# Kernel optimization log

Hardware: AMD Instinct MI355X
Metric: run time of the kernel (lower is better)

Reference implementation:

```python
import jax, jax.numpy as jnp
import numpy as np
import math

N_RES, N_EDGE = 10000, 320000
C_S, C_Z, C_H, H, PQ, PV = 384, 128, 16, 12, 4, 8
INF, EPS = 1e5, 1e-8


def _lin(key, din, dout):
    k1, k2 = jax.random.split(key)
    w = jax.random.normal(k1, (din, dout), jnp.float32) * (1.0 / np.sqrt(din))
    b = jax.random.normal(k2, (dout,), jnp.float32) * 0.02
    return w, b


def setup_inputs() -> dict:
    key = jax.random.key(0)
    ks = jax.random.split(key, 16)
    s = jax.random.normal(ks[0], (N_RES, C_S), jnp.float32)
    z = jax.random.normal(ks[1], (N_EDGE, C_Z), jnp.float32)
    edge_index = jax.random.randint(ks[2], (2, N_EDGE), 0, N_RES, jnp.int32)
    rot = jnp.linalg.qr(jax.random.normal(ks[3], (N_RES, 3, 3), jnp.float32))[0]
    trans = jax.random.normal(ks[4], (N_RES, 3), jnp.float32)
    mask = jnp.ones((N_RES,), jnp.float32)
    wq, bq = _lin(ks[5], C_S, H * C_H)
    wkv, bkv = _lin(ks[6], C_S, 2 * H * C_H)
    wqp, bqp = _lin(ks[7], C_S, H * PQ * 3)
    wkvp, bkvp = _lin(ks[8], C_S, H * (PQ + PV) * 3)
    wb, bb = _lin(ks[9], C_Z, H)
    wdz, bdz = _lin(ks[10], C_Z, C_Z // 4)
    head_w = jax.random.normal(ks[11], (H,), jnp.float32) * 0.1
    wout, bout = _lin(ks[12], H * (C_Z // 4 + C_H + PV * 4), C_S)
    return dict(s=s, z=z, rot=rot, trans=trans, mask=mask, edge_index=edge_index,
                wq=wq, bq=bq, wkv=wkv, bkv=bkv, wqp=wqp, bqp=bqp, wkvp=wkvp, bkvp=bkvp,
                wb=wb, bb=bb, wdz=wdz, bdz=bdz, head_w=head_w, wout=wout, bout=bout)


def reference(s, z, rot, trans, mask, edge_index, wq, bq, wkv, bkv, wqp, bqp,
              wkvp, bkvp, wb, bb, wdz, bdz, head_w, wout, bout):
    n = s.shape[0]
    src, dst = edge_index[0], edge_index[1]  # key-side, query-side

    q = (s @ wq + bq).reshape(n, H, C_H)
    kv = (s @ wkv + bkv).reshape(n, H, 2 * C_H)
    k, v = kv[..., :C_H], kv[..., C_H:]

    def make_pts(x, p):
        # torch: split [n, H*p*3] into 3 chunks of H*p, stack on last dim -> [n, H*p, 3]
        x = jnp.stack(jnp.split(x, 3, axis=-1), axis=-1)
        x = jnp.einsum('nij,npj->npi', rot, x) + trans[:, None, :]  # global frame
        return x.reshape(n, H, p, 3)

    q_pts = make_pts(s @ wqp + bqp, PQ)                 # [n, H, PQ, 3]
    kv_pts = make_pts(s @ wkvp + bkvp, PQ + PV)
    k_pts, v_pts = kv_pts[..., :PQ, :], kv_pts[..., PQ:, :]

    b = z @ wb + bb                                      # [E, H]
    a = jnp.einsum('ehc,ehc->eh', q[dst], k[src]) * math.sqrt(1.0 / (3 * C_H))
    a = a + math.sqrt(1.0 / 3) * b

    disp = q_pts[dst] - k_pts[src]                       # [E, H, PQ, 3]
    hw = jax.nn.softplus(head_w) * math.sqrt(1.0 / (3 * (PQ * 9.0 / 2)))
    pt_att = -0.5 * jnp.einsum('ehp,h->eh', jnp.sum(disp * disp, axis=-1), hw)

    edge_mask = INF * (mask[src] * mask[dst] - 1.0)
    a = a + pt_att + edge_mask[:, None]

    # segment softmax over edges grouped by destination node
    m = jax.lax.stop_gradient(jax.ops.segment_max(a, dst, num_segments=n))
    ea = jnp.exp(a - m[dst])
    a = ea / (jax.ops.segment_sum(ea, dst, num_segments=n)[dst] + 1e-16)

    o = jax.ops.segment_sum(a[..., None] * v[src], dst, num_segments=n).reshape(n, -1)

    o_pt = jax.ops.segment_sum(a[..., None, None] * v_pts[src], dst, num_segments=n)  # [n,H,PV,3]
    o_pt = jnp.einsum('nji,nhpj->nhpi', rot, o_pt - trans[:, None, None, :])  # invert_apply
    o_pt_norm = jnp.sqrt(jnp.sum(o_pt * o_pt, axis=-1) + EPS).reshape(n, -1)
    o_pt = o_pt.reshape(n, H * PV, 3)

    pair_z = z @ wdz + bdz                               # [E, c_z//4]
    o_pair = jax.ops.segment_sum(a[..., None] * pair_z[:, None, :], dst,
                                 num_segments=n).reshape(n, -1)

    feats = jnp.concatenate([o, o_pt[..., 0], o_pt[..., 1], o_pt[..., 2],
                             o_pt_norm, o_pair], axis=-1)
    return feats @ wout + bout
```

## Files before the change

kernel.cpp:

```cpp
#include <hip/hip_runtime.h>
#include <hip/hip_bf16.h>
#include <math.h>

#define N_RESC 10000
#define N_EDGEC 320000
#define C_SC 384
#define C_ZC 128
#define AGG_D 864
#define FEAT_D 960
#define OUT_D 384

#define S1C 0.14433756729740643f
#define S2C 0.5773502691896258f
#define SHWC 0.13608276348795434f

__global__ void k_zero(int* cursor) {
    int i = blockIdx.x * 256 + threadIdx.x;
    if (i < N_RESC) cursor[i] = 0;
}

__global__ void k_hist(const int* __restrict__ ei, int* cursor) {
    int e = blockIdx.x * 256 + threadIdx.x;
    if (e < N_EDGEC) atomicAdd(&cursor[ei[N_EDGEC + e]], 1);
}

__global__ __launch_bounds__(1024) void k_scan(int* cursor, int* rowptr) {
    __shared__ int buf[1024];
    __shared__ int carry_s;
    int t = threadIdx.x;
    if (t == 0) carry_s = 0;
    __syncthreads();
    for (int ch = 0; ch < 10; ++ch) {
        int idx = ch * 1024 + t;
        int v = (idx < N_RESC) ? cursor[idx] : 0;
        buf[t] = v;
        __syncthreads();
        for (int off = 1; off < 1024; off <<= 1) {
            int x = (t >= off) ? buf[t - off] : 0;
            __syncthreads();
            buf[t] += x;
            __syncthreads();
        }
        int incl = buf[t];
        int excl = incl - v;
        int base = carry_s;
        int total = buf[1023];
        if (idx < N_RESC) { rowptr[idx] = base + excl; cursor[idx] = base + excl; }
        __syncthreads();
        if (t == 0) carry_s = base + total;
        __syncthreads();
    }
    if (t == 0) rowptr[N_RESC] = carry_s;
}

__global__ void k_scatter(const int* __restrict__ ei, int* cursor, int* csr,
                          int* src_csr, int* epos) {
    int e = blockIdx.x * 256 + threadIdx.x;
    if (e < N_EDGEC) {
        int d = ei[N_EDGEC + e];
        int s = ei[e];
        int pos = atomicAdd(&cursor[d], 1);
        csr[pos] = e;
        src_csr[pos] = s;
        epos[e] = pos;
    }
}

__global__ __launch_bounds__(256) void k_wpack(
    const float* __restrict__ wq, const float* __restrict__ bq,
    const float* __restrict__ wkv, const float* __restrict__ bkv,
    const float* __restrict__ wqp, const float* __restrict__ bqp,
    const float* __restrict__ wkvp, const float* __restrict__ bkvp,
    const float* __restrict__ wb, const float* __restrict__ bb,
    const float* __restrict__ wdz, const float* __restrict__ bdz,
    float* __restrict__ wpack, float* __restrict__ bpack,
    float* __restrict__ wzpack, float* __restrict__ bzpack) {
    int idx = blockIdx.x * 256 + threadIdx.x;
    if (idx < 384 * 1152) {
        int j = idx / 1152, c = idx % 1152;
        float v;
        if (c < 192)      v = wq[j * 192 + c];
        else if (c < 576) v = wkv[j * 384 + (c - 192)];
        else if (c < 720) v = wqp[j * 144 + (c - 576)];
        else              v = wkvp[j * 432 + (c - 720)];
        wpack[idx] = v;
    }
    if (idx < 1152) {
        float b;
        if (idx < 192)      b = bq[idx];
        else if (idx < 576) b = bkv[idx - 192];
        else if (idx < 720) b = bqp[idx - 576];
        else                b = bkvp[idx - 720];
        bpack[idx] = b;
    }
    if (idx < 128 * 48) {
        int j = idx / 48, c = idx % 48;
        float v = 0.f;
        if (c < 12)      v = wb[j * 12 + c];
        else if (c < 44) v = wdz[j * 32 + (c - 12)];
        wzpack[idx] = v;
    }
    if (idx < 48) {
        float b = 0.f;
        if (idx < 12)      b = bb[idx];
        else if (idx < 44) b = bdz[idx - 12];
        bzpack[idx] = b;
    }
}

#define BM 64
#define BN 128
#define BK 32
__global__ __launch_bounds__(256) void k_proj(const float* __restrict__ s,
    const float* __restrict__ wpack, const float* __restrict__ bpack,
    float* __restrict__ qh, float* __restrict__ kh, float* __restrict__ vh,
    float* __restrict__ praw) {
    __shared__ float sT[BK][BM + 4];
    __shared__ float wt[BK][BN];
    int t = threadIdx.x;
    int bm0 = blockIdx.x * BM;
    int bn0 = blockIdx.y * BN;
    int tcol = t & 31;
    int trow = t >> 5;
    int c0 = tcol * 4;
    int r0 = trow * 8;

    int srow = t >> 2;
    int skoff = (t & 3) * 8;
    int gsrow = min(bm0 + srow, N_RESC - 1);
    const float* srcp = s + (long)gsrow * C_SC + skoff;

    float acc[8][4];
    #pragma unroll
    for (int i = 0; i < 8; i++)
        #pragma unroll
        for (int j = 0; j < 4; j++) acc[i][j] = 0.f;

    for (int k0 = 0; k0 < C_SC; k0 += BK) {
        float4 sa = *(const float4*)(srcp + k0);
        float4 sb = *(const float4*)(srcp + k0 + 4);
        sT[skoff + 0][srow] = sa.x; sT[skoff + 1][srow] = sa.y;
        sT[skoff + 2][srow] = sa.z; sT[skoff + 3][srow] = sa.w;
        sT[skoff + 4][srow] = sb.x; sT[skoff + 5][srow] = sb.y;
        sT[skoff + 6][srow] = sb.z; sT[skoff + 7][srow] = sb.w;
        #pragma unroll
        for (int q = 0; q < 4; q++) {
            int kk = (t >> 5) + q * 8;
            *(float4*)&wt[kk][c0] =
                *(const float4*)(wpack + (long)(k0 + kk) * 1152 + bn0 + c0);
        }
        __syncthreads();
        #pragma unroll
        for (int k = 0; k < BK; k++) {
            float4 a0 = *(const float4*)&sT[k][r0];
            float4 a1 = *(const float4*)&sT[k][r0 + 4];
            float4 b  = *(const float4*)&wt[k][c0];
            float av0 = a0.x, av1 = a0.y, av2 = a0.z, av3 = a0.w;
            float av4 = a1.x, av5 = a1.y, av6 = a1.z, av7 = a1.w;
            acc[0][0] = fmaf(av0, b.x, acc[0][0]); acc[0][1] = fmaf(av0, b.y, acc[0][1]);
            acc[0][2] = fmaf(av0, b.z, acc[0][2]); acc[0][3] = fmaf(av0, b.w, acc[0][3]);
            acc[1][0] = fmaf(av1, b.x, acc[1][0]); acc[1][1] = fmaf(av1, b.y, acc[1][1]);
            acc[1][2] = fmaf(av1, b.z, acc[1][2]); acc[1][3] = fmaf(av1, b.w, acc[1][3]);
            acc[2][0] = fmaf(av2, b.x, acc[2][0]); acc[2][1] = fmaf(av2, b.y, acc[2][1]);
            acc[2][2] = fmaf(av2, b.z, acc[2][2]); acc[2][3] = fmaf(av2, b.w, acc[2][3]);
            acc[3][0] = fmaf(av3, b.x, acc[3][0]); acc[3][1] = fmaf(av3, b.y, acc[3][1]);
            acc[3][2] = fmaf(av3, b.z, acc[3][2]); acc[3][3] = fmaf(av3, b.w, acc[3][3]);
            acc[4][0] = fmaf(av4, b.x, acc[4][0]); acc[4][1] = fmaf(av4, b.y, acc[4][1]);
            acc[4][2] = fmaf(av4, b.z, acc[4][2]); acc[4][3] = fmaf(av4, b.w, acc[4][3]);
            acc[5][0] = fmaf(av5, b.x, acc[5][0]); acc[5][1] = fmaf(av5, b.y, acc[5][1]);
            acc[5][2] = fmaf(av5, b.z, acc[5][2]); acc[5][3] = fmaf(av5, b.w, acc[5][3]);
            acc[6][0] = fmaf(av6, b.x, acc[6][0]); acc[6][1] = fmaf(av6, b.y, acc[6][1]);
            acc[6][2] = fmaf(av6, b.z, acc[6][2]); acc[6][3] = fmaf(av6, b.w, acc[6][3]);
            acc[7][0] = fmaf(av7, b.x, acc[7][0]); acc[7][1] = fmaf(av7, b.y, acc[7][1]);
            acc[7][2] = fmaf(av7, b.z, acc[7][2]); acc[7][3] = fmaf(av7, b.w, acc[7][3]);
        }
        __syncthreads();
    }
    #pragma unroll
    for (int j = 0; j < 4; j++) {
        int c = bn0 + c0 + j;
        float bv = bpack[c];
        #pragma unroll
        for (int i = 0; i < 8; i++) {
            int n = bm0 + r0 + i;
            if (n < N_RESC) {
                float val = acc[i][j] + bv;
                if (c < 192) qh[(long)n * 192 + c] = val;
                else if (c < 576) {
                    int cc = c - 192; int h = cc >> 5, r = cc & 31;
                    if (r < 16) kh[(long)n * 192 + h * 16 + r] = val;
                    else        vh[(long)n * 192 + h * 16 + (r - 16)] = val;
                } else praw[(long)n * 576 + (c - 576)] = val;
            }
        }
    }
}

__global__ __launch_bounds__(192) void k_rot(const float* __restrict__ praw,
    const float* __restrict__ rot, const float* __restrict__ trans,
    float* __restrict__ qpts, float* __restrict__ kpts, float* __restrict__ vpts) {
    int n = blockIdx.x;
    int t = threadIdx.x;
    __shared__ float R[9], T[3];
    if (t < 9) R[t] = rot[n * 9 + t];
    if (t < 3) T[t] = trans[n * 3 + t];
    __syncthreads();
    const float* pr = praw + (long)n * 576;
    if (t < 48) {
        float x0 = pr[t], x1 = pr[48 + t], x2 = pr[96 + t];
        #pragma unroll
        for (int i = 0; i < 3; i++)
            qpts[(long)n * 144 + t * 3 + i] = R[i*3+0]*x0 + R[i*3+1]*x1 + R[i*3+2]*x2 + T[i];
    } else {
        int p = t - 48;
        float x0 = pr[144 + p], x1 = pr[288 + p], x2 = pr[432 + p];
        int h = p / 12, pp = p % 12;
        #pragma unroll
        for (int i = 0; i < 3; i++) {
            float val = R[i*3+0]*x0 + R[i*3+1]*x1 + R[i*3+2]*x2 + T[i];
            if (pp < 4) kpts[(long)n * 144 + (h * 4 + pp) * 3 + i] = val;
            else        vpts[(long)n * 288 + (h * 8 + (pp - 4)) * 3 + i] = val;
        }
    }
}

#define ZBM 128
__global__ __launch_bounds__(256) void k_zproj(const float* __restrict__ z,
    const int* __restrict__ epos,
    const float* __restrict__ wzpack, const float* __restrict__ bzpack,
    float* __restrict__ b_e, float* __restrict__ pairz) {
    __shared__ float zT[32][ZBM + 4];
    __shared__ float wl[128][48];
    int t = threadIdx.x;
    long e0 = (long)blockIdx.x * ZBM;
    int er = t & 31;
    int cg = t >> 5;
    int cb = cg * 6;

    #pragma unroll
    for (int q = 0; q < 6; q++) {
        int f = t + q * 256;
        int row = f / 12, c4 = f % 12;
        *(float4*)&wl[row][c4 * 4] = *(const float4*)(wzpack + row * 48 + c4 * 4);
    }

    float acc[4][6];
    #pragma unroll
    for (int i = 0; i < 4; i++)
        #pragma unroll
        for (int j = 0; j < 6; j++) acc[i][j] = 0.f;

    int r = t >> 1, ch2 = t & 1;
    const float* zp = z + (e0 + r) * C_ZC + ch2 * 16;

    for (int kc = 0; kc < 4; kc++) {
        __syncthreads();
        #pragma unroll
        for (int q = 0; q < 4; q++) {
            float4 v = *(const float4*)(zp + kc * 32 + q * 4);
            int kk = ch2 * 16 + q * 4;
            zT[kk + 0][r] = v.x; zT[kk + 1][r] = v.y;
            zT[kk + 2][r] = v.z; zT[kk + 3][r] = v.w;
        }
        __syncthreads();
        #pragma unroll
        for (int k = 0; k < 32; k++) {
            float4 zv = *(const float4*)&zT[k][er * 4];
            const float* wrow = &wl[kc * 32 + k][cb];
            float w0 = wrow[0], w1 = wrow[1], w2 = wrow[2];
            float w3 = wrow[3], w4 = wrow[4], w5 = wrow[5];
            acc[0][0] = fmaf(zv.x, w0, acc[0][0]); acc[0][1] = fmaf(zv.x, w1, acc[0][1]);
            acc[0][2] = fmaf(zv.x, w2, acc[0][2]); acc[0][3] = fmaf(zv.x, w3, acc[0][3]);
            acc[0][4] = fmaf(zv.x, w4, acc[0][4]); acc[0][5] = fmaf(zv.x, w5, acc[0][5]);
            acc[1][0] = fmaf(zv.y, w0, acc[1][0]); acc[1][1] = fmaf(zv.y, w1, acc[1][1]);
            acc[1][2] = fmaf(zv.y, w2, acc[1][2]); acc[1][3] = fmaf(zv.y, w3, acc[1][3]);
            acc[1][4] = fmaf(zv.y, w4, acc[1][4]); acc[1][5] = fmaf(zv.y, w5, acc[1][5]);
            acc[2][0] = fmaf(zv.z, w0, acc[2][0]); acc[2][1] = fmaf(zv.z, w1, acc[2][1]);
            acc[2][2] = fmaf(zv.z, w2, acc[2][2]); acc[2][3] = fmaf(zv.z, w3, acc[2][3]);
            acc[2][4] = fmaf(zv.z, w4, acc[2][4]); acc[2][5] = fmaf(zv.z, w5, acc[2][5]);
            acc[3][0] = fmaf(zv.w, w0, acc[3][0]); acc[3][1] = fmaf(zv.w, w1, acc[3][1]);
            acc[3][2] = fmaf(zv.w, w2, acc[3][2]); acc[3][3] = fmaf(zv.w, w3, acc[3][3]);
            acc[3][4] = fmaf(zv.w, w4, acc[3][4]); acc[3][5] = fmaf(zv.w, w5, acc[3][5]);
        }
    }

    float bz0 = bzpack[cb + 0], bz1 = bzpack[cb + 1], bz2 = bzpack[cb + 2];
    float bz3 = bzpack[cb + 3], bz4 = bzpack[cb + 4], bz5 = bzpack[cb + 5];
    #pragma unroll
    for (int ei = 0; ei < 4; ei++) {
        long pos = epos[e0 + er * 4 + ei];
        float o0 = acc[ei][0] + bz0, o1 = acc[ei][1] + bz1;
        float o2 = acc[ei][2] + bz2, o3 = acc[ei][3] + bz3;
        float o4 = acc[ei][4] + bz4, o5 = acc[ei][5] + bz5;
        if (cb < 12) {
            float* d = b_e + pos * 12 + cb;
            *(float2*)(d + 0) = make_float2(o0, o1);
            *(float2*)(d + 2) = make_float2(o2, o3);
            *(float2*)(d + 4) = make_float2(o4, o5);
        } else if (cb < 42) {
            float* d = pairz + pos * 32 + (cb - 12);
            *(float2*)(d + 0) = make_float2(o0, o1);
            *(float2*)(d + 2) = make_float2(o2, o3);
            *(float2*)(d + 4) = make_float2(o4, o5);
        } else {
            *(float2*)(pairz + pos * 32 + 30) = make_float2(o0, o1);
        }
    }
}

#define CAPA 256
__global__ __launch_bounds__(256) void k_attn(const int* __restrict__ rowptr,
    const int* __restrict__ src_csr,
    const float* __restrict__ qh, const float* __restrict__ kh,
    const float* __restrict__ qpts, const float* __restrict__ kpts,
    const float* __restrict__ mask, const float* __restrict__ head_w,
    const float* __restrict__ b_e,
    const float* __restrict__ vh, const float* __restrict__ vpts,
    const float* __restrict__ pairz,
    float* __restrict__ agg) {
    int n = blockIdx.x;
    int t = threadIdx.x;
    __shared__ float qf[192], qp[144], hws[12];
    __shared__ int slist[CAPA];
    __shared__ float al[CAPA * 12];
    __shared__ float red[16 * 12];
    __shared__ float mh[12], lh[12], rh[12];
    if (t < 192) qf[t] = qh[(long)n * 192 + t];
    if (t < 144) qp[t] = qpts[(long)n * 144 + t];
    if (t < 12) { hws[t] = log1pf(expf(head_w[t])) * SHWC; mh[t] = -1e30f; lh[t] = 0.f; }
    float mdst = mask[n];
    int row0 = rowptr[n];
    int deg = rowptr[n + 1] - row0;
    int w = t >> 6, l = t & 63, c = l & 15, hq = l >> 4;
    int g = t >> 4, l16 = t & 15;

    const float* base = nullptr;
    int scale = 0, hk = 0, use_e = 0;
    int comp = t * 4;
    if (comp < 192)      { base = vh + comp; scale = 192; hk = comp >> 4; }
    else if (comp < 480) { int idx = comp - 192; base = vpts + idx; scale = 288; hk = idx / 24; }
    else if (comp < 864) { int idx = comp - 480; base = pairz + (idx & 31); scale = 32; hk = idx >> 5; use_e = 1; }
    float4 acc = make_float4(0.f, 0.f, 0.f, 0.f);

    for (int cs = 0; cs < deg; cs += CAPA) {
        int cnt = min(CAPA, deg - cs);
        int p0 = row0 + cs;
        __syncthreads();
        for (int i = t; i < cnt; i += 256) slist[i] = src_csr[p0 + i];
        __syncthreads();
        for (int i = w * 2; i < cnt; i += 8) {
            int i1 = min(i + 1, cnt - 1);
            int s0 = slist[i], s1 = slist[i1];
            float em0 = 100000.0f * (mask[s0] * mdst - 1.0f);
            float em1 = 100000.0f * (mask[s1] * mdst - 1.0f);
            float kv0[3], kv1[3];
            #pragma unroll
            for (int tp = 0; tp < 3; tp++) {
                kv0[tp] = kh[(long)s0 * 192 + tp * 64 + l];
                kv1[tp] = kh[(long)s1 * 192 + tp * 64 + l];
            }
            float kp0[3] = {0.f,0.f,0.f}, kp1[3] = {0.f,0.f,0.f};
            if (c < 12) {
                #pragma unroll
                for (int tp = 0; tp < 3; tp++) {
                    int h = tp * 4 + hq;
                    kp0[tp] = kpts[(long)s0 * 144 + h * 12 + c];
                    kp1[tp] = kpts[(long)s1 * 144 + h * 12 + c];
                }
            }
            float be0[3] = {0.f,0.f,0.f}, be1[3] = {0.f,0.f,0.f};
            if (c == 0) {
                #pragma unroll
                for (int tp = 0; tp < 3; tp++) {
                    int h = tp * 4 + hq;
                    be0[tp] = b_e[(long)(p0 + i) * 12 + h];
                    be1[tp] = b_e[(long)(p0 + i1) * 12 + h];
                }
            }
            #pragma unroll
            for (int tp = 0; tp < 3; tp++) {
                int h = tp * 4 + hq;
                float qfv = S1C * qf[h * 16 + c];
                float val0 = qfv * kv0[tp];
                float val1 = qfv * kv1[tp];
                if (c < 12) {
                    float qpv = qp[h * 12 + c];
                    float hw = -0.5f * hws[h];
                    float d0 = qpv - kp0[tp];
                    float d1 = qpv - kp1[tp];
                    val0 = fmaf(hw * d0, d0, val0);
                    val1 = fmaf(hw * d1, d1, val1);
                }
                val0 += __shfl_xor(val0, 8, 16); val1 += __shfl_xor(val1, 8, 16);
                val0 += __shfl_xor(val0, 4, 16); val1 += __shfl_xor(val1, 4, 16);
                val0 += __shfl_xor(val0, 2, 16); val1 += __shfl_xor(val1, 2, 16);
                val0 += __shfl_xor(val0, 1, 16); val1 += __shfl_xor(val1, 1, 16);
                if (c == 0) {
                    al[i * 12 + h] = val0 + S2C * be0[tp] + em0;
                    if (i1 != i)
                        al[i1 * 12 + h] = val1 + S2C * be1[tp] + em1;
                }
            }
        }
        __syncthreads();
        if (l16 < 12) {
            float lm = -1e30f;
            for (int i = g; i < cnt; i += 16) lm = fmaxf(lm, al[i * 12 + l16]);
            red[g * 12 + l16] = lm;
        }
        __syncthreads();
        if (t < 12) {
            float m = mh[t];
            for (int gg = 0; gg < 16; gg++) m = fmaxf(m, red[gg * 12 + t]);
            rh[t] = expf(mh[t] - m);
            mh[t] = m;
        }
        __syncthreads();
        if (l16 < 12) {
            float m = mh[l16];
            float ls = 0.f;
            for (int i = g; i < cnt; i += 16) {
                float p = expf(al[i * 12 + l16] - m);
                al[i * 12 + l16] = p;
                ls += p;
            }
            red[g * 12 + l16] = ls;
        }
        __syncthreads();
        if (t < 12) {
            float ss = 0.f;
            for (int gg = 0; gg < 16; gg++) ss += red[gg * 12 + t];
            lh[t] = lh[t] * rh[t] + ss;
        }
        __syncthreads();
        if (t < 216) {
            float r = rh[hk];
            acc.x *= r; acc.y *= r; acc.z *= r; acc.w *= r;
            int i = 0;
            for (; i + 4 <= cnt; i += 4) {
                int i0 = use_e ? (p0 + i)     : slist[i];
                int i1 = use_e ? (p0 + i + 1) : slist[i+1];
                int i2 = use_e ? (p0 + i + 2) : slist[i+2];
                int i3 = use_e ? (p0 + i + 3) : slist[i+3];
                float4 v0 = *(const float4*)(base + (long)i0 * scale);
                float4 v1 = *(const float4*)(base + (long)i1 * scale);
                float4 v2 = *(const float4*)(base + (long)i2 * scale);
                float4 v3 = *(const float4*)(base + (long)i3 * scale);
                float w0 = al[i * 12 + hk];
                float w1 = al[(i+1) * 12 + hk];
                float w2 = al[(i+2) * 12 + hk];
                float w3 = al[(i+3) * 12 + hk];
                acc.x = fmaf(w0, v0.x, acc.x); acc.y = fmaf(w0, v0.y, acc.y);
                acc.z = fmaf(w0, v0.z, acc.z); acc.w = fmaf(w0, v0.w, acc.w);
                acc.x = fmaf(w1, v1.x, acc.x); acc.y = fmaf(w1, v1.y, acc.y);
                acc.z = fmaf(w1, v1.z, acc.z); acc.w = fmaf(w1, v1.w, acc.w);
                acc.x = fmaf(w2, v2.x, acc.x); acc.y = fmaf(w2, v2.y, acc.y);
                acc.z = fmaf(w2, v2.z, acc.z); acc.w = fmaf(w2, v2.w, acc.w);
                acc.x = fmaf(w3, v3.x, acc.x); acc.y = fmaf(w3, v3.y, acc.y);
                acc.z = fmaf(w3, v3.z, acc.z); acc.w = fmaf(w3, v3.w, acc.w);
            }
            for (; i < cnt; i++) {
                int ii = use_e ? (p0 + i) : slist[i];
                float4 v = *(const float4*)(base + (long)ii * scale);
                float wv = al[i * 12 + hk];
                acc.x = fmaf(wv, v.x, acc.x); acc.y = fmaf(wv, v.y, acc.y);
                acc.z = fmaf(wv, v.z, acc.z); acc.w = fmaf(wv, v.w, acc.w);
            }
        }
    }
    if (t < 216) {
        float linv = 1.f / (lh[hk] + 1e-16f);
        acc.x *= linv; acc.y *= linv; acc.z *= linv; acc.w *= linv;
        *(float4*)(agg + (long)n * AGG_D + comp) = acc;
    }
}

#define NT_F 8
__global__ __launch_bounds__(192) void k_feat(const float* __restrict__ agg,
    const float* __restrict__ rot, const float* __restrict__ trans,
    float* __restrict__ feats) {
    int t = threadIdx.x;
    int node0 = blockIdx.x * NT_F;
    for (int idx = t; idx < NT_F * 192; idx += 192) {
        int nt = idx / 192, c = idx % 192;
        feats[(long)(node0 + nt) * FEAT_D + c] = agg[(long)(node0 + nt) * AGG_D + c];
    }
    for (int idx = t; idx < NT_F * 96; idx += 192) {
        int nt = idx / 96, p = idx % 96;
        int n = node0 + nt;
        const float* a = agg + (long)n * AGG_D;
        float gx = a[192 + p * 3 + 0] - trans[n * 3 + 0];
        float gy = a[192 + p * 3 + 1] - trans[n * 3 + 1];
        float gz = a[192 + p * 3 + 2] - trans[n * 3 + 2];
        const float* R = rot + (long)n * 9;
        float lx = R[0] * gx + R[3] * gy + R[6] * gz;
        float ly = R[1] * gx + R[4] * gy + R[7] * gz;
        float lz = R[2] * gx + R[5] * gy + R[8] * gz;
        float* f = feats + (long)n * FEAT_D;
        f[192 + p] = lx;
        f[288 + p] = ly;
        f[384 + p] = lz;
        f[480 + p] = sqrtf(lx * lx + ly * ly + lz * lz + 1e-8f);
    }
    for (int idx = t; idx < NT_F * 384; idx += 192) {
        int nt = idx / 384, q = idx % 384;
        feats[(long)(node0 + nt) * FEAT_D + 576 + q] =
            agg[(long)(node0 + nt) * AGG_D + 480 + q];
    }
}

__global__ __launch_bounds__(256) void k_out(const float* __restrict__ feats,
    const float* __restrict__ wout, const float* __restrict__ bout,
    float* __restrict__ out) {
    __shared__ float sT[BK][BM + 4];
    __shared__ float wt[BK][BN];
    int t = threadIdx.x;
    int bm0 = blockIdx.x * BM;
    int bn0 = blockIdx.y * BN;
    int tcol = t & 31;
    int trow = t >> 5;
    int c0 = tcol * 4;
    int r0 = trow * 8;

    int srow = t >> 2;
    int skoff = (t & 3) * 8;
    int gsrow = min(bm0 + srow, N_RESC - 1);
    const float* srcp = feats + (long)gsrow * FEAT_D + skoff;

    float acc[8][4];
    #pragma unroll
    for (int i = 0; i < 8; i++)
        #pragma unroll
        for (int j = 0; j < 4; j++) acc[i][j] = 0.f;

    for (int k0 = 0; k0 < FEAT_D; k0 += BK) {
        float4 sa = *(const float4*)(srcp + k0);
        float4 sb = *(const float4*)(srcp + k0 + 4);
        sT[skoff + 0][srow] = sa.x; sT[skoff + 1][srow] = sa.y;
        sT[skoff + 2][srow] = sa.z; sT[skoff + 3][srow] = sa.w;
        sT[skoff + 4][srow] = sb.x; sT[skoff + 5][srow] = sb.y;
        sT[skoff + 6][srow] = sb.z; sT[skoff + 7][srow] = sb.w;
        #pragma unroll
        for (int q = 0; q < 4; q++) {
            int kk = (t >> 5) + q * 8;
            *(float4*)&wt[kk][c0] =
                *(const float4*)(wout + (long)(k0 + kk) * OUT_D + bn0 + c0);
        }
        __syncthreads();
        #pragma unroll
        for (int k = 0; k < BK; k++) {
            float4 a0 = *(const float4*)&sT[k][r0];
            float4 a1 = *(const float4*)&sT[k][r0 + 4];
            float4 b  = *(const float4*)&wt[k][c0];
            float av0 = a0.x, av1 = a0.y, av2 = a0.z, av3 = a0.w;
            float av4 = a1.x, av5 = a1.y, av6 = a1.z, av7 = a1.w;
            acc[0][0] = fmaf(av0, b.x, acc[0][0]); acc[0][1] = fmaf(av0, b.y, acc[0][1]);
            acc[0][2] = fmaf(av0, b.z, acc[0][2]); acc[0][3] = fmaf(av0, b.w, acc[0][3]);
            acc[1][0] = fmaf(av1, b.x, acc[1][0]); acc[1][1] = fmaf(av1, b.y, acc[1][1]);
            acc[1][2] = fmaf(av1, b.z, acc[1][2]); acc[1][3] = fmaf(av1, b.w, acc[1][3]);
            acc[2][0] = fmaf(av2, b.x, acc[2][0]); acc[2][1] = fmaf(av2, b.y, acc[2][1]);
            acc[2][2] = fmaf(av2, b.z, acc[2][2]); acc[2][3] = fmaf(av2, b.w, acc[2][3]);
            acc[3][0] = fmaf(av3, b.x, acc[3][0]); acc[3][1] = fmaf(av3, b.y, acc[3][1]);
            acc[3][2] = fmaf(av3, b.z, acc[3][2]); acc[3][3] = fmaf(av3, b.w, acc[3][3]);
            acc[4][0] = fmaf(av4, b.x, acc[4][0]); acc[4][1] = fmaf(av4, b.y, acc[4][1]);
            acc[4][2] = fmaf(av4, b.z, acc[4][2]); acc[4][3] = fmaf(av4, b.w, acc[4][3]);
            acc[5][0] = fmaf(av5, b.x, acc[5][0]); acc[5][1] = fmaf(av5, b.y, acc[5][1]);
            acc[5][2] = fmaf(av5, b.z, acc[5][2]); acc[5][3] = fmaf(av5, b.w, acc[5][3]);
            acc[6][0] = fmaf(av6, b.x, acc[6][0]); acc[6][1] = fmaf(av6, b.y, acc[6][1]);
            acc[6][2] = fmaf(av6, b.z, acc[6][2]); acc[6][3] = fmaf(av6, b.w, acc[6][3]);
            acc[7][0] = fmaf(av7, b.x, acc[7][0]); acc[7][1] = fmaf(av7, b.y, acc[7][1]);
            acc[7][2] = fmaf(av7, b.z, acc[7][2]); acc[7][3] = fmaf(av7, b.w, acc[7][3]);
        }
        __syncthreads();
    }
    float bv0 = bout[bn0 + c0 + 0];
    float bv1 = bout[bn0 + c0 + 1];
    float bv2 = bout[bn0 + c0 + 2];
    float bv3 = bout[bn0 + c0 + 3];
    #pragma unroll
    for (int i = 0; i < 8; i++) {
        int n = bm0 + r0 + i;
        if (n < N_RESC) {
            *(float4*)(out + (long)n * OUT_D + bn0 + c0) =
                make_float4(acc[i][0] + bv0, acc[i][1] + bv1,
                            acc[i][2] + bv2, acc[i][3] + bv3);
        }
    }
}

extern "C" void kernel_launch(void* const* d_in, const int* in_sizes, int n_in,
                              void* d_out, int out_size, void* d_ws, size_t ws_size,
                              hipStream_t stream) {
    const float* s     = (const float*)d_in[0];
    const float* z     = (const float*)d_in[1];
    const float* rot   = (const float*)d_in[2];
    const float* trans = (const float*)d_in[3];
    const float* mask  = (const float*)d_in[4];
    const int*   ei    = (const int*)d_in[5];
    const float* wq    = (const float*)d_in[6];
    const float* bq    = (const float*)d_in[7];
    const float* wkv   = (const float*)d_in[8];
    const float* bkv   = (const float*)d_in[9];
    const float* wqp   = (const float*)d_in[10];
    const float* bqp   = (const float*)d_in[11];
    const float* wkvp  = (const float*)d_in[12];
    const float* bkvp  = (const float*)d_in[13];
    const float* wb    = (const float*)d_in[14];
    const float* bb    = (const float*)d_in[15];
    const float* wdz   = (const float*)d_in[16];
    const float* bdz   = (const float*)d_in[17];
    const float* head_w= (const float*)d_in[18];
    const float* wout  = (const float*)d_in[19];
    const float* bout  = (const float*)d_in[20];
    float* out = (float*)d_out;

    float* ws    = (float*)d_ws;
    float* qh    = ws;
    float* kh    = qh + 1920000;
    float* vh    = kh + 1920000;
    float* qpts  = vh + 1920000;
    float* kpts  = qpts + 1440000;
    float* vpts  = kpts + 1440000;
    float* b_e   = vpts + 2880000;
    float* pairz = b_e + 3840000;
    float* alog  = pairz + 10240000;
    float* agg   = alog + 3840000;
    float* praw  = agg;
    float* wpack = agg + 5760000;
    float* bpack = wpack + 442368;
    float* wzpack= bpack + 1152;
    float* bzpack= wzpack + 6144;
    float* feats = pairz;
    int* rowptr  = (int*)(agg + 8640000);
    int* cursor  = rowptr + 10004;
    int* csr     = cursor + 10000;
    int* src_csr = csr + N_EDGEC;
    int* epos    = src_csr + N_EDGEC;

    k_zero<<<(N_RESC + 255) / 256, 256, 0, stream>>>(cursor);
    k_hist<<<(N_EDGEC + 255) / 256, 256, 0, stream>>>(ei, cursor);
    k_scan<<<1, 1024, 0, stream>>>(cursor, rowptr);
    k_scatter<<<(N_EDGEC + 255) / 256, 256, 0, stream>>>(ei, cursor, csr, src_csr, epos);

    k_wpack<<<(384 * 1152 + 255) / 256, 256, 0, stream>>>(wq, bq, wkv, bkv, wqp, bqp,
                                                          wkvp, bkvp, wb, bb, wdz, bdz,
                                                          wpack, bpack, wzpack, bzpack);
    dim3 pgrid((N_RESC + BM - 1) / BM, 1152 / BN);
    k_proj<<<pgrid, 256, 0, stream>>>(s, wpack, bpack, qh, kh, vh, praw);
    k_rot<<<N_RESC, 192, 0, stream>>>(praw, rot, trans, qpts, kpts, vpts);

    k_zproj<<<N_EDGEC / ZBM, 256, 0, stream>>>(z, epos, wzpack, bzpack, b_e, pairz);

    k_attn<<<N_RESC, 256, 0, stream>>>(rowptr, src_csr, qh, kh, qpts, kpts,
                                       mask, head_w, b_e, vh, vpts, pairz, agg);

    k_feat<<<N_RESC / NT_F, 192, 0, stream>>>(agg, rot, trans, feats);
    dim3 ogrid((N_RESC + BM - 1) / BM, OUT_D / BN);
    k_out<<<ogrid, 256, 0, stream>>>(feats, wout, bout, out);
}
```

Measured before the change: 767.1 us.

## Fuse frame-inversion feature build into attention kernel; shrink output GEMM tile

Result: no change. 765.7 us (-0.2%).

```diff
diff --git a/kernel.cpp b/kernel.cpp
--- a/kernel.cpp
+++ b/kernel.cpp
@@ -308,7 +308,7 @@
     }
 }
 
-#define CAPA 256
+#define CAPA 64
 __global__ __launch_bounds__(256) void k_attn(const int* __restrict__ rowptr,
     const int* __restrict__ src_csr,
     const float* __restrict__ qh, const float* __restrict__ kh,
@@ -317,7 +317,8 @@
     const float* __restrict__ b_e,
     const float* __restrict__ vh, const float* __restrict__ vpts,
     const float* __restrict__ pairz,
-    float* __restrict__ agg) {
+    const float* __restrict__ rot, const float* __restrict__ trans,
+    float* __restrict__ feats) {
     int n = blockIdx.x;
     int t = threadIdx.x;
     __shared__ float qf[192], qp[144], hws[12];
@@ -325,9 +326,13 @@
     __shared__ float al[CAPA * 12];
     __shared__ float red[16 * 12];
     __shared__ float mh[12], lh[12], rh[12];
+    __shared__ float aggl[AGG_D];
+    __shared__ float R[9], T[3];
     if (t < 192) qf[t] = qh[(long)n * 192 + t];
     if (t < 144) qp[t] = qpts[(long)n * 144 + t];
     if (t < 12) { hws[t] = log1pf(expf(head_w[t])) * SHWC; mh[t] = -1e30f; lh[t] = 0.f; }
+    if (t >= 192 && t < 201) R[t - 192] = rot[(long)n * 9 + (t - 192)];
+    if (t >= 204 && t < 207) T[t - 204] = trans[(long)n * 3 + (t - 204)];
     float mdst = mask[n];
     int row0 = rowptr[n];
     int deg = rowptr[n + 1] - row0;
@@ -468,78 +473,62 @@
             }
         }
     }
+    __syncthreads();
     if (t < 216) {
         float linv = 1.f / (lh[hk] + 1e-16f);
-        acc.x *= linv; acc.y *= linv; acc.z *= linv; acc.w *= linv;
-        *(float4*)(agg + (long)n * AGG_D + comp) = acc;
-    }
-}
-
-#define NT_F 8
-__global__ __launch_bounds__(192) void k_feat(const float* __restrict__ agg,
-    const float* __restrict__ rot, const float* __restrict__ trans,
-    float* __restrict__ feats) {
-    int t = threadIdx.x;
-    int node0 = blockIdx.x * NT_F;
-    for (int idx = t; idx < NT_F * 192; idx += 192) {
-        int nt = idx / 192, c = idx % 192;
-        feats[(long)(node0 + nt) * FEAT_D + c] = agg[(long)(node0 + nt) * AGG_D + c];
-    }
-    for (int idx = t; idx < NT_F * 96; idx += 192) {
-        int nt = idx / 96, p = idx % 96;
-        int n = node0 + nt;
-        const float* a = agg + (long)n * AGG_D;
-        float gx = a[192 + p * 3 + 0] - trans[n * 3 + 0];
-        float gy = a[192 + p * 3 + 1] - trans[n * 3 + 1];
-        float gz = a[192 + p * 3 + 2] - trans[n * 3 + 2];
-        const float* R = rot + (long)n * 9;
+        aggl[comp + 0] = acc.x * linv;
+        aggl[comp + 1] = acc.y * linv;
+        aggl[comp + 2] = acc.z * linv;
+        aggl[comp + 3] = acc.w * linv;
+    }
+    __syncthreads();
+    float* f = feats + (long)n * FEAT_D;
+    if (t < 192) f[t] = aggl[t];
+    if (t < 96) {
+        int p = t;
+        float gx = aggl[192 + p * 3 + 0] - T[0];
+        float gy = aggl[192 + p * 3 + 1] - T[1];
+        float gz = aggl[192 + p * 3 + 2] - T[2];
         float lx = R[0] * gx + R[3] * gy + R[6] * gz;
         float ly = R[1] * gx + R[4] * gy + R[7] * gz;
         float lz = R[2] * gx + R[5] * gy + R[8] * gz;
-        float* f = feats + (long)n * FEAT_D;
         f[192 + p] = lx;
         f[288 + p] = ly;
         f[384 + p] = lz;
         f[480 + p] = sqrtf(lx * lx + ly * ly + lz * lz + 1e-8f);
     }
-    for (int idx = t; idx < NT_F * 384; idx += 192) {
-        int nt = idx / 384, q = idx % 384;
-        feats[(long)(node0 + nt) * FEAT_D + 576 + q] =
-            agg[(long)(node0 + nt) * AGG_D + 480 + q];
-    }
-}
-
+    for (int q = t; q < 384; q += 256) f[576 + q] = aggl[480 + q];
+}
+
+#define OBM 32
 __global__ __launch_bounds__(256) void k_out(const float* __restrict__ feats,
     const float* __restrict__ wout, const float* __restrict__ bout,
     float* __restrict__ out) {
-    __shared__ float sT[BK][BM + 4];
+    __shared__ float sT[BK][OBM + 4];
     __shared__ float wt[BK][BN];
     int t = threadIdx.x;
-    int bm0 = blockIdx.x * BM;
+    int bm0 = blockIdx.x * OBM;
     int bn0 = blockIdx.y * BN;
     int tcol = t & 31;
     int trow = t >> 5;
     int c0 = tcol * 4;
-    int r0 = trow * 8;
-
-    int srow = t >> 2;
-    int skoff = (t & 3) * 8;
+    int r0 = trow * 4;
+
+    int srow = t >> 3;
+    int skoff = (t & 7) * 4;
     int gsrow = min(bm0 + srow, N_RESC - 1);
     const float* srcp = feats + (long)gsrow * FEAT_D + skoff;
 
-    float acc[8][4];
+    float acc[4][4];
     #pragma unroll
-    for (int i = 0; i < 8; i++)
+    for (int i = 0; i < 4; i++)
         #pragma unroll
         for (int j = 0; j < 4; j++) acc[i][j] = 0.f;
 
     for (int k0 = 0; k0 < FEAT_D; k0 += BK) {
         float4 sa = *(const float4*)(srcp + k0);
-        float4 sb = *(const float4*)(srcp + k0 + 4);
         sT[skoff + 0][srow] = sa.x; sT[skoff + 1][srow] = sa.y;
         sT[skoff + 2][srow] = sa.z; sT[skoff + 3][srow] = sa.w;
-        sT[skoff + 4][srow] = sb.x; sT[skoff + 5][srow] = sb.y;
-        sT[skoff + 6][srow] = sb.z; sT[skoff + 7][srow] = sb.w;
         #pragma unroll
         for (int q = 0; q < 4; q++) {
             int kk = (t >> 5) + q * 8;
@@ -550,10 +539,8 @@
         #pragma unroll
         for (int k = 0; k < BK; k++) {
             float4 a0 = *(const float4*)&sT[k][r0];
-            float4 a1 = *(const float4*)&sT[k][r0 + 4];
             float4 b  = *(const float4*)&wt[k][c0];
             float av0 = a0.x, av1 = a0.y, av2 = a0.z, av3 = a0.w;
-            float av4 = a1.x, av5 = a1.y, av6 = a1.z, av7 = a1.w;
             acc[0][0] = fmaf(av0, b.x, acc[0][0]); acc[0][1] = fmaf(av0, b.y, acc[0][1]);
             acc[0][2] = fmaf(av0, b.z, acc[0][2]); acc[0][3] = fmaf(av0, b.w, acc[0][3]);
             acc[1][0] = fmaf(av1, b.x, acc[1][0]); acc[1][1] = fmaf(av1, b.y, acc[1][1]);
@@ -562,14 +549,6 @@
             acc[2][2] = fmaf(av2, b.z, acc[2][2]); acc[2][3] = fmaf(av2, b.w, acc[2][3]);
             acc[3][0] = fmaf(av3, b.x, acc[3][0]); acc[3][1] = fmaf(av3, b.y, acc[3][1]);
             acc[3][2] = fmaf(av3, b.z, acc[3][2]); acc[3][3] = fmaf(av3, b.w, acc[3][3]);
-            acc[4][0] = fmaf(av4, b.x, acc[4][0]); acc[4][1] = fmaf(av4, b.y, acc[4][1]);
-            acc[4][2] = fmaf(av4, b.z, acc[4][2]); acc[4][3] = fmaf(av4, b.w, acc[4][3]);
-            acc[5][0] = fmaf(av5, b.x, acc[5][0]); acc[5][1] = fmaf(av5, b.y, acc[5][1]);
-            acc[5][2] = fmaf(av5, b.z, acc[5][2]); acc[5][3] = fmaf(av5, b.w, acc[5][3]);
-            acc[6][0] = fmaf(av6, b.x, acc[6][0]); acc[6][1] = fmaf(av6, b.y, acc[6][1]);
-            acc[6][2] = fmaf(av6, b.z, acc[6][2]); acc[6][3] = fmaf(av6, b.w, acc[6][3]);
-            acc[7][0] = fmaf(av7, b.x, acc[7][0]); acc[7][1] = fmaf(av7, b.y, acc[7][1]);
-            acc[7][2] = fmaf(av7, b.z, acc[7][2]); acc[7][3] = fmaf(av7, b.w, acc[7][3]);
         }
         __syncthreads();
     }
@@ -578,7 +557,7 @@
     float bv2 = bout[bn0 + c0 + 2];
     float bv3 = bout[bn0 + c0 + 3];
     #pragma unroll
-    for (int i = 0; i < 8; i++) {
+    for (int i = 0; i < 4; i++) {
         int n = bm0 + r0 + i;
         if (n < N_RESC) {
             *(float4*)(out + (long)n * OUT_D + bn0 + c0) =
@@ -625,12 +604,12 @@
     float* pairz = b_e + 3840000;
     float* alog  = pairz + 10240000;
     float* agg   = alog + 3840000;
+    float* feats = alog;
     float* praw  = agg;
     float* wpack = agg + 5760000;
     float* bpack = wpack + 442368;
     float* wzpack= bpack + 1152;
     float* bzpack= wzpack + 6144;
-    float* feats = pairz;
     int* rowptr  = (int*)(agg + 8640000);
     int* cursor  = rowptr + 10004;
     int* csr     = cursor + 10000;
@@ -652,9 +631,9 @@
     k_zproj<<<N_EDGEC / ZBM, 256, 0, stream>>>(z, epos, wzpack, bzpack, b_e, pairz);
 
     k_attn<<<N_RESC, 256, 0, stream>>>(rowptr, src_csr, qh, kh, qpts, kpts,
-                                       mask, head_w, b_e, vh, vpts, pairz, agg);
-
-    k_feat<<<N_RESC / NT_F, 192, 0, stream>>>(agg, rot, trans, feats);
-    dim3 ogrid((N_RESC + BM - 1) / BM, OUT_D / BN);
+                                       mask, head_w, b_e, vh, vpts, pairz,
+                                       rot, trans, feats);
+
+    dim3 ogrid((N_RESC + OBM - 1) / OBM, OUT_D / BN);
     k_out<<<ogrid, 256, 0, stream>>>(feats, wout, bout, out);
 }
```
